# Performance work log

Hardware: AMD Instinct MI355X
Metric: run time of the kernel (lower is better)

Reference implementation:

```python
import jax, jax.numpy as jnp
import numpy as np

# symmetry-function hyperparameters (match module defaults), meshgrid order as in TF code
_LAMBD_INIT = np.array([1.0, -1.0])
_ITA_INIT = np.array([4.0])
_ZETA_INIT = np.array([2.0, 4.0, 8.0])
_lg, _ig, _zg = np.meshgrid(_LAMBD_INIT, _ITA_INIT, _ZETA_INIT)
LAMBD = jnp.asarray(_lg.flatten(), dtype=jnp.float32)  # [L], L = 6
ITA = jnp.asarray(_ig.flatten(), dtype=jnp.float32)
ZETA = jnp.asarray(_zg.flatten(), dtype=jnp.float32)

B, M = 16, 64  # batch, max_atoms


def setup_inputs() -> dict:
    key = jax.random.key(0)
    k1, k2, k3 = jax.random.split(key, 3)
    d_cutoff = jax.random.uniform(k1, (B, M, M), dtype=jnp.float32)
    d = jax.random.uniform(k2, (B, M, M), dtype=jnp.float32)
    atom_coordinates = jax.random.normal(k3, (B, M, 3), dtype=jnp.float32)
    return {"d_cutoff": d_cutoff, "d": d, "atom_coordinates": atom_coordinates}


def reference(d_cutoff, d, atom_coordinates):
    # pairwise displacement vectors: [B, M, M, 3]
    vec = atom_coordinates[:, :, None, :] - atom_coordinates[:, None, :, :]
    # broadcastable triple-distance views [B, M(i), M(j), M(k)]
    R_ij = d[:, :, :, None]
    R_ik = d[:, :, None, :]
    R_jk = d[:, None, :, :]
    # theta = (r_ij . r_ik) / (R_ij * R_ik + eps)   (cosine ratio; original then takes cos of it)
    theta = jnp.einsum('bijd,bikd->bijk', vec, vec) / (R_ij * R_ik + 1e-5)
    sum_sq = R_ij * R_ij + R_ik * R_ik + R_jk * R_jk  # [B, M, M, M]
    f_prod = (d_cutoff[:, :, :, None] * d_cutoff[:, :, None, :]
              * d_cutoff[:, None, :, :])  # [B, M, M, M]
    lambd = LAMBD.reshape(1, 1, 1, 1, -1)
    ita = ITA.reshape(1, 1, 1, 1, -1)
    zeta = ZETA.reshape(1, 1, 1, 1, -1)
    # faithful to original: cos is applied to the cosine ratio itself
    out = (jnp.power(1.0 + lambd * jnp.cos(theta)[..., None], zeta)
           * jnp.exp(-ita * sum_sq[..., None])
           * f_prod[..., None])  # [B, M, M, M, L]
    res = out.sum(axis=(2, 3)) * jnp.power(jnp.float32(2.0), 1.0 - ZETA.reshape(1, 1, -1))
    return res  # [B, M, L]
```

## Files before the change

### kernel.cpp

```cpp
#include <hip/hip_runtime.h>
#include <hip/hip_bf16.h>
#include <math.h>


#define BB 16
#define MM 64
#define PP 6

__device__ __forceinline__ float fast_cos(float x) {
    double xd = (double)x;
    double fn = rint(xd * 0.63661977236758138243);
    float  r  = (float)fma(-fn, 1.5707963267948966, xd);
    int    q  = ((int)fn) & 3;
    float  z  = r * r;
    float s = r + r * z * (-1.6666666641626524e-01f + z * (8.3333293858894632e-03f
              + z * (-1.9839334836096632e-04f + z * 2.7183114939898219e-06f)));
    float c = 1.0f + z * (-4.9999999725103100e-01f + z * (4.1666623323739063e-02f
              + z * (-1.3886763774609929e-03f + z * 2.4390448796277409e-05f)));
    float mag = (q & 1) ? s : c;
    return __int_as_float(__float_as_int(mag) ^ (((q + 1) & 2) << 30));
}

__device__ __forceinline__ void accum_powers(float c, float w,
    float& a0, float& a1, float& a2, float& a3, float& a4, float& a5) {
    float u = 1.0f + c, v = 1.0f - c;
    float u2 = u * u,  v2 = v * v;
    float u4 = u2 * u2, v4 = v2 * v2;
    float u8 = u4 * u4, v8 = v4 * v4;
    a0 += u2 * w; a1 += u4 * w; a2 += u8 * w;
    a3 += v2 * w; a4 += v4 * w; a5 += v8 * w;
}

__global__ __launch_bounds__(256) void angsym_kernel(
    const float* __restrict__ d_cutoff,
    const float* __restrict__ d,
    const float* __restrict__ coords,
    float* __restrict__ out)
{
    __shared__ float4 Vrow[MM];
    __shared__ float  Arow[MM];
    __shared__ float  Tmat[MM * MM];
    __shared__ float  red[4 * PP];

    const int blk = blockIdx.x;
    const int b = blk >> 6;
    const int i = blk & 63;
    const int t = threadIdx.x;

    const float* __restrict__ db = d        + b * MM * MM;
    const float* __restrict__ cb = d_cutoff + b * MM * MM;

    if (t < MM) {
        const float* cc = coords + b * MM * 3;
        float dv = db[i * MM + t];
        Arow[t] = expf(-4.0f * dv * dv) * cb[i * MM + t];
        Vrow[t] = make_float4(cc[i * 3 + 0] - cc[t * 3 + 0],
                              cc[i * 3 + 1] - cc[t * 3 + 1],
                              cc[i * 3 + 2] - cc[t * 3 + 2],
                              dv);
    }
    __syncthreads();

    #pragma unroll
    for (int s = 0; s < (MM * MM) / 256; ++s) {
        int idx = t + s * 256;
        int j = idx >> 6, k = idx & 63;
        float dv = db[idx];
        float g  = expf(-4.0f * dv * dv) * cb[idx];
        Tmat[idx] = g * Arow[j] * Arow[k];
    }
    __syncthreads();

    const int hl = t & 31;
    const int g  = t >> 5;

    float a0 = 0.f, a1 = 0.f, a2 = 0.f, a3 = 0.f, a4 = 0.f, a5 = 0.f;

    #pragma unroll
    for (int s = 0; s < 8; ++s) {
        const int r = g + (s << 3);
        if (r >= 63) continue;
        int p1, p2;
        if (hl == 0) { p1 = 63; p2 = r; }
        else {
            p1 = r + hl; if (p1 >= 63) p1 -= 63;
            p2 = r - hl; if (p2 < 0)   p2 += 63;
        }
        float4 Vj = Vrow[p1];
        float4 Vk = Vrow[p2];
        float dot = Vj.x * Vk.x + Vj.y * Vk.y + Vj.z * Vk.z;
        float den = Vj.w * Vk.w + 1e-5f;
        float c   = fast_cos(dot / den);
        float w   = Tmat[p1 * MM + p2] + Tmat[p2 * MM + p1];
        accum_powers(c, w, a0, a1, a2, a3, a4, a5);
    }

    if (t < MM) {
        float4 Vd = Vrow[t];
        float dot = Vd.x * Vd.x + Vd.y * Vd.y + Vd.z * Vd.z;
        float den = Vd.w * Vd.w + 1e-5f;
        float c   = fast_cos(dot / den);
        float w   = Tmat[t * MM + t];
        accum_powers(c, w, a0, a1, a2, a3, a4, a5);
    }

    #pragma unroll
    for (int off = 32; off > 0; off >>= 1) {
        a0 += __shfl_down(a0, off);
        a1 += __shfl_down(a1, off);
        a2 += __shfl_down(a2, off);
        a3 += __shfl_down(a3, off);
        a4 += __shfl_down(a4, off);
        a5 += __shfl_down(a5, off);
    }

    const int wave = t >> 6;
    const int lane = t & 63;
    if (lane == 0) {
        red[wave * PP + 0] = a0;
        red[wave * PP + 1] = a1;
        red[wave * PP + 2] = a2;
        red[wave * PP + 3] = a3;
        red[wave * PP + 4] = a4;
        red[wave * PP + 5] = a5;
    }
    __syncthreads();

    if (t < PP) {
        float s = red[t] + red[PP + t] + red[2 * PP + t] + red[3 * PP + t];
        const float scale = (t % 3 == 0) ? 0.5f : ((t % 3 == 1) ? 0.125f : 0.0078125f);
        out[(b * MM + i) * PP + t] = s * scale;
    }
}

extern "C" void kernel_launch(void* const* d_in, const int* in_sizes, int n_in,
                              void* d_out, int out_size, void* d_ws, size_t ws_size,
                              hipStream_t stream) {
    const float* d_cutoff = (const float*)d_in[0];
    const float* d        = (const float*)d_in[1];
    const float* coords   = (const float*)d_in[2];
    float* out            = (float*)d_out;

    angsym_kernel<<<BB * MM, 256, 0, stream>>>(d_cutoff, d, coords, out);
}
```

Before: 63.89 us.

## Use 512 threads, float4 loads of distance matrices, and float32 range reduction in cos

Doubles the block to 512 threads, so each thread handles half as many (j,k) pairs and the cross-wave reduction covers eight waves. The d and d_cutoff matrices are loaded as float4 into registers before the first barrier, and Tmat is built with vectorized shared-memory stores. The cos range reduction switches from double to a two-step float Cody-Waite reduction to avoid FP64 ops. It risks slightly lower precision for large arguments and lower occupancy per block.

```diff
diff --git a/kernel.cpp b/kernel.cpp
--- a/kernel.cpp
+++ b/kernel.cpp
@@ -8,11 +8,11 @@
 #define PP 6
 
 __device__ __forceinline__ float fast_cos(float x) {
-    double xd = (double)x;
-    double fn = rint(xd * 0.63661977236758138243);
-    float  r  = (float)fma(-fn, 1.5707963267948966, xd);
-    int    q  = ((int)fn) & 3;
-    float  z  = r * r;
+    float fn = rintf(x * 0.63661977236758134308f);
+    float r  = fmaf(-fn, 1.57079637050628662109375f, x);
+    r        = fmaf(-fn, -4.37113900018624283e-08f, r);
+    int    q = ((int)fn) & 3;
+    float  z = r * r;
     float s = r + r * z * (-1.6666666641626524e-01f + z * (8.3333293858894632e-03f
               + z * (-1.9839334836096632e-04f + z * 2.7183114939898219e-06f)));
     float c = 1.0f + z * (-4.9999999725103100e-01f + z * (4.1666623323739063e-02f
@@ -31,16 +31,16 @@
     a3 += v2 * w; a4 += v4 * w; a5 += v8 * w;
 }
 
-__global__ __launch_bounds__(256) void angsym_kernel(
+__global__ __launch_bounds__(512) void angsym_kernel(
     const float* __restrict__ d_cutoff,
     const float* __restrict__ d,
     const float* __restrict__ coords,
     float* __restrict__ out)
 {
     __shared__ float4 Vrow[MM];
-    __shared__ float  Arow[MM];
-    __shared__ float  Tmat[MM * MM];
-    __shared__ float  red[4 * PP];
+    __shared__ __align__(16) float Arow[MM];
+    __shared__ __align__(16) float Tmat[MM * MM];
+    __shared__ float red[8 * PP];
 
     const int blk = blockIdx.x;
     const int b = blk >> 6;
@@ -49,6 +49,11 @@
 
     const float* __restrict__ db = d        + b * MM * MM;
     const float* __restrict__ cb = d_cutoff + b * MM * MM;
+
+    const float4* __restrict__ db4 = (const float4*)db;
+    const float4* __restrict__ cb4 = (const float4*)cb;
+    float4 dq0 = db4[t],       cq0 = cb4[t];
+    float4 dq1 = db4[t + 512], cq1 = cb4[t + 512];
 
     if (t < MM) {
         const float* cc = coords + b * MM * 3;
@@ -62,12 +67,20 @@
     __syncthreads();
 
     #pragma unroll
-    for (int s = 0; s < (MM * MM) / 256; ++s) {
-        int idx = t + s * 256;
-        int j = idx >> 6, k = idx & 63;
-        float dv = db[idx];
-        float g  = expf(-4.0f * dv * dv) * cb[idx];
-        Tmat[idx] = g * Arow[j] * Arow[k];
+    for (int s = 0; s < 2; ++s) {
+        const int v = t + s * 512;
+        const float4 dv = s ? dq1 : dq0;
+        const float4 cv = s ? cq1 : cq0;
+        const int j  = v >> 4;
+        const int kb = (v & 15) << 2;
+        const float  aj = Arow[j];
+        const float4 ak = *(const float4*)&Arow[kb];
+        float4 tv;
+        tv.x = expf(-4.0f * dv.x * dv.x) * cv.x * aj * ak.x;
+        tv.y = expf(-4.0f * dv.y * dv.y) * cv.y * aj * ak.y;
+        tv.z = expf(-4.0f * dv.z * dv.z) * cv.z * aj * ak.z;
+        tv.w = expf(-4.0f * dv.w * dv.w) * cv.w * aj * ak.w;
+        ((float4*)Tmat)[v] = tv;
     }
     __syncthreads();
 
@@ -77,8 +90,8 @@
     float a0 = 0.f, a1 = 0.f, a2 = 0.f, a3 = 0.f, a4 = 0.f, a5 = 0.f;
 
     #pragma unroll
-    for (int s = 0; s < 8; ++s) {
-        const int r = g + (s << 3);
+    for (int s = 0; s < 4; ++s) {
+        const int r = g + (s << 4);
         if (r >= 63) continue;
         int p1, p2;
         if (hl == 0) { p1 = 63; p2 = r; }
@@ -127,7 +140,8 @@
     __syncthreads();
 
     if (t < PP) {
-        float s = red[t] + red[PP + t] + red[2 * PP + t] + red[3 * PP + t];
+        float s = red[t]          + red[PP + t]     + red[2 * PP + t] + red[3 * PP + t]
+                + red[4 * PP + t] + red[5 * PP + t] + red[6 * PP + t] + red[7 * PP + t];
         const float scale = (t % 3 == 0) ? 0.5f : ((t % 3 == 1) ? 0.125f : 0.0078125f);
         out[(b * MM + i) * PP + t] = s * scale;
     }
@@ -141,5 +155,5 @@
     const float* coords   = (const float*)d_in[2];
     float* out            = (float*)d_out;
 
-    angsym_kernel<<<BB * MM, 256, 0, stream>>>(d_cutoff, d, coords, out);
+    angsym_kernel<<<BB * MM, 512, 0, stream>>>(d_cutoff, d, coords, out);
 }
```

Result: no change. 63.87 us (-0.0%).
